# Kernel tuning notes

Measured on AMD Instinct MI355X. Metric: run time of the kernel, lower is better.

## Reference

```python
import jax, jax.numpy as jnp
import numpy as np

N = 100_000   # nodes
E = 3_200_000 # edges (avg degree 32)
F = 256       # in_features == out_features


def setup_inputs() -> dict:
    key = jax.random.key(0)
    k1, k2, k3, k4, k5, k6 = jax.random.split(key, 6)
    x = jax.random.normal(k1, (N, F), dtype=jnp.float32)
    h0 = jax.random.normal(k2, (N, F), dtype=jnp.float32)
    adj_rows = jax.random.randint(k3, (E,), 0, N, dtype=jnp.int32)
    adj_cols = jax.random.randint(k4, (E,), 0, N, dtype=jnp.int32)
    # roughly row-normalized adjacency values (avg degree 32)
    adj_vals = jax.random.uniform(k5, (E,), dtype=jnp.float32) / 32.0
    stdv = 1.0 / np.sqrt(F)
    weight = jax.random.uniform(k6, (F, F), dtype=jnp.float32, minval=-stdv, maxval=stdv)
    return {"x": x, "adj_rows": adj_rows, "adj_cols": adj_cols, "adj_vals": adj_vals,
            "h0": h0, "weight": weight, "lamda": 0.5, "alpha": 0.1, "l": 4}


def reference(x, adj_rows, adj_cols, adj_vals, h0, weight, lamda, alpha, l):
    # theta = log(lamda/l + 1)
    theta = jnp.log(jnp.float32(lamda) / l + 1.0)
    # hi = sparse.mm(adj, x): gather source rows, scale by edge value, scatter-add to dest rows
    hi = jax.ops.segment_sum(adj_vals[:, None] * x[adj_cols], adj_rows, num_segments=x.shape[0])  # [N, F]
    # support == 1 branch: affine blend with initial features h0
    support = (1.0 - alpha) * hi + alpha * h0
    # output = theta * support @ W + (1 - theta) * support   (residual=False)
    return theta * (support @ weight) + (1.0 - theta) * support
```

## Files before the change

kernel.cpp:

```cpp
#include <hip/hip_runtime.h>
#include <math.h>

#define F 256

#define BKT_SHIFT 7
#define BKT_ROWS 128
#define BKT_CAP 8192
#define NB_MAX 1024
#define BIN_CHUNK 8192

typedef __attribute__((ext_vector_type(8))) short short8;
typedef __attribute__((ext_vector_type(4))) float f32x4;
typedef __attribute__((ext_vector_type(2))) int i32x2;
typedef __attribute__((ext_vector_type(4))) unsigned short u16x4;
typedef __attribute__((ext_vector_type(8))) unsigned short u16x8;

__device__ __forceinline__ unsigned short f2bf(float f) {
  union { float f; unsigned u; } v; v.f = f;
  unsigned r = (v.u + 0x7fffu + ((v.u >> 16) & 1u)) >> 16;
  return (unsigned short)r;
}
__device__ __forceinline__ float bf2f(unsigned short h) {
  union { unsigned u; float f; } v; v.u = ((unsigned)h) << 16;
  return v.f;
}

__global__ void prep(const float* __restrict__ W, unsigned short* __restrict__ Wt,
                     const float* __restrict__ x, unsigned short* __restrict__ xb,
                     int NF, int do_xb) {
  if (blockIdx.x < 256) {
    int idx = blockIdx.x * 256 + threadIdx.x;
    int k = idx >> 8, n = idx & 255;
    Wt[n * F + k] = f2bf(W[k * F + n]);
    return;
  }
  if (!do_xb) return;
  int i0 = (blockIdx.x - 256) * 2048 + threadIdx.x * 8;
  if (i0 + 8 <= NF) {
    f32x4 a = __builtin_nontemporal_load((const f32x4*)(x + i0));
    f32x4 b = __builtin_nontemporal_load((const f32x4*)(x + i0 + 4));
    u16x8 o;
    o[0] = f2bf(a.x); o[1] = f2bf(a.y); o[2] = f2bf(a.z); o[3] = f2bf(a.w);
    o[4] = f2bf(b.x); o[5] = f2bf(b.y); o[6] = f2bf(b.z); o[7] = f2bf(b.w);
    *(u16x8*)(xb + i0) = o;
  } else {
    for (int i = i0; i < NF; ++i) xb[i] = f2bf(x[i]);
  }
}

__global__ void hist_rows(const int* __restrict__ rows, int* counts, int E) {
  int e = blockIdx.x * 256 + threadIdx.x;
  if (e < E) atomicAdd(&counts[__builtin_nontemporal_load(&rows[e])], 1);
}

__global__ void scan1(const int* __restrict__ counts, int* row_start, int* blk, int N) {
  __shared__ int tmp[256];
  int t = threadIdx.x;
  int i = blockIdx.x * 256 + t;
  int v = (i < N) ? counts[i] : 0;
  tmp[t] = v;
  __syncthreads();
#pragma unroll
  for (int off = 1; off < 256; off <<= 1) {
    int a = (t >= off) ? tmp[t - off] : 0;
    __syncthreads();
    tmp[t] += a;
    __syncthreads();
  }
  if (i < N) row_start[i] = tmp[t] - v;
  if (t == 255) blk[blockIdx.x] = tmp[255];
}

__global__ void scan2(int* blk, int NB) {
  __shared__ int tmp[512];
  int t = threadIdx.x;
  int v = (t < NB) ? blk[t] : 0;
  tmp[t] = v;
  __syncthreads();
#pragma unroll
  for (int off = 1; off < 512; off <<= 1) {
    int a = (t >= off) ? tmp[t - off] : 0;
    __syncthreads();
    tmp[t] += a;
    __syncthreads();
  }
  if (t < NB) blk[t] = tmp[t] - v;
}

__global__ void scan3(const int* __restrict__ counts, int* row_start,
                      const int* __restrict__ blk, int* fill_ptr, int N) {
  int i = blockIdx.x * 256 + threadIdx.x;
  if (i >= N) return;
  int rs = row_start[i] + blk[i >> 8];
  row_start[i] = rs;
  fill_ptr[i] = rs;
  if (i == N - 1) row_start[N] = rs + counts[i];
}

__global__ void fill_csr(const int* __restrict__ rows, const int* __restrict__ cols,
                         const float* __restrict__ vals, int* fill_ptr,
                         int2* __restrict__ edges, int E) {
  int e = blockIdx.x * 256 + threadIdx.x;
  if (e >= E) return;
  int r = __builtin_nontemporal_load(&rows[e]);
  int c = __builtin_nontemporal_load(&cols[e]);
  float v = __builtin_nontemporal_load(&vals[e]);
  int pos = atomicAdd(&fill_ptr[r], 1);
  edges[pos] = make_int2(c, __float_as_int(v));
}

__global__ __launch_bounds__(512) void bin_count(
    const int* __restrict__ rows, int* __restrict__ bucket_counts, int E, int NB) {
  __shared__ unsigned hist[NB_MAX];
  const int tid = threadIdx.x;
  const int e0 = blockIdx.x * BIN_CHUNK;
  for (int b = tid; b < NB; b += 512) hist[b] = 0;
  __syncthreads();
#pragma unroll
  for (int k = 0; k < BIN_CHUNK / 512; ++k) {
    int e = e0 + k * 512 + tid;
    if (e < E) {
      unsigned b = (unsigned)__builtin_nontemporal_load(&rows[e]) >> BKT_SHIFT;
      atomicAdd(&hist[b], 1u);
    }
  }
  __syncthreads();
  for (int b = tid; b < NB; b += 512)
    if (hist[b]) atomicAdd(&bucket_counts[b], (int)hist[b]);
}

__global__ __launch_bounds__(1024) void scan_buckets(
    const int* __restrict__ bucket_counts, int* __restrict__ bbase,
    int* __restrict__ bcur, int* __restrict__ row_start, int NB, int N, int E) {
  __shared__ int tmp[1024];
  int t = threadIdx.x;
  int v = (t < NB) ? bucket_counts[t] : 0;
  tmp[t] = v;
  __syncthreads();
#pragma unroll
  for (int off = 1; off < 1024; off <<= 1) {
    int a = (t >= off) ? tmp[t - off] : 0;
    __syncthreads();
    tmp[t] += a;
    __syncthreads();
  }
  if (t < NB) {
    int ex = tmp[t] - v;
    bbase[t] = ex;
    bcur[t] = ex;
  }
  if (t == 0) {
    bbase[NB] = E;
    row_start[N] = E;
  }
}

__global__ __launch_bounds__(512) void bin_edges(
    const int* __restrict__ rows, const int* __restrict__ cols,
    const float* __restrict__ vals, int* __restrict__ bcur,
    i32x2* __restrict__ etmp, int E, int NB) {
  __shared__ unsigned hist[NB_MAX];
  __shared__ unsigned base[NB_MAX];
  const int tid = threadIdx.x;
  const int e0 = blockIdx.x * BIN_CHUNK;

  for (int b = tid; b < NB; b += 512) hist[b] = 0;
  __syncthreads();
#pragma unroll
  for (int k = 0; k < BIN_CHUNK / 512; ++k) {
    int e = e0 + k * 512 + tid;
    if (e < E) {
      unsigned b = (unsigned)__builtin_nontemporal_load(&rows[e]) >> BKT_SHIFT;
      atomicAdd(&hist[b], 1u);
    }
  }
  __syncthreads();
  for (int b = tid; b < NB; b += 512) {
    unsigned c = hist[b];
    base[b] = c ? (unsigned)atomicAdd(&bcur[b], (int)c) : 0u;
    hist[b] = 0;
  }
  __syncthreads();
#pragma unroll
  for (int k = 0; k < BIN_CHUNK / 512; ++k) {
    int e = e0 + k * 512 + tid;
    if (e < E) {
      int r = rows[e];
      unsigned b = (unsigned)r >> BKT_SHIFT;
      unsigned idx = atomicAdd(&hist[b], 1u);
      int pos = (int)(base[b] + idx);
      int c = cols[e];
      float v = vals[e];
      etmp[pos] = (i32x2){c | ((r & (BKT_ROWS - 1)) << 20), __float_as_int(v)};
    }
  }
}

__global__ __launch_bounds__(512) void sort_bucket(
    const i32x2* __restrict__ etmp, const int* __restrict__ bbase,
    i32x2* __restrict__ edges, int* __restrict__ row_start, int N) {
  __shared__ int cur[BKT_ROWS];
  __shared__ int pre[BKT_ROWS];
  __shared__ i32x2 sorted[BKT_CAP];
  const int b = blockIdx.x;
  const int r0 = b << BKT_SHIFT;
  int nrows = N - r0; if (nrows > BKT_ROWS) nrows = BKT_ROWS;
  const int seg0 = bbase[b];
  const int cnt = bbase[b + 1] - seg0;
  const int tid = threadIdx.x;

  if (tid < BKT_ROWS) cur[tid] = 0;
  __syncthreads();
  for (int i = tid; i < cnt; i += 512) {
    i32x2 w = etmp[seg0 + i];
    atomicAdd(&cur[(w.x >> 20) & (BKT_ROWS - 1)], 1);
  }
  __syncthreads();
  int myc = (tid < BKT_ROWS) ? cur[tid] : 0;
  __syncthreads();
  for (int off = 1; off < BKT_ROWS; off <<= 1) {
    int a = 0;
    if (tid < BKT_ROWS && tid >= off) a = cur[tid - off];
    __syncthreads();
    if (tid < BKT_ROWS) cur[tid] += a;
    __syncthreads();
  }
  if (tid < BKT_ROWS) {
    int ex = cur[tid] - myc;
    pre[tid] = ex;
    cur[tid] = ex;
    if (tid < nrows) row_start[r0 + tid] = seg0 + ex;
  }
  __syncthreads();

  if (cnt <= BKT_CAP) {
    for (int i = tid; i < cnt; i += 512) {
      i32x2 w = etmp[seg0 + i];
      int rl = (w.x >> 20) & (BKT_ROWS - 1);
      int idx = atomicAdd(&cur[rl], 1);
      sorted[idx] = (i32x2){w.x & 0xFFFFF, w.y};
    }
    __syncthreads();
    for (int i = tid; i < cnt; i += 512)
      edges[seg0 + i] = sorted[i];
  } else {
    for (int i = tid; i < cnt; i += 512) {
      i32x2 w = etmp[seg0 + i];
      int rl = (w.x >> 20) & (BKT_ROWS - 1);
      int idx = atomicAdd(&cur[rl], 1);
      edges[seg0 + idx] = (i32x2){w.x & 0xFFFFF, w.y};
    }
  }
}

__global__ __launch_bounds__(256) void gather_rows_bf16(
    const unsigned short* __restrict__ xb, const float* __restrict__ h0,
    const int* __restrict__ row_start, const i32x2* __restrict__ edges,
    float* __restrict__ support, const float* __restrict__ alpha_p, int N) {
  int gid = blockIdx.x * 256 + threadIdx.x;
  int r = gid >> 6;
  if (r >= N) return;
  int lane = threadIdx.x & 63;
  float alpha = *alpha_p;
  int s = row_start[r], e = row_start[r + 1];

  const unsigned short* xbl = xb + lane * 4;

  f32x4 acc0 = (f32x4){0.f, 0.f, 0.f, 0.f};
  f32x4 acc1 = (f32x4){0.f, 0.f, 0.f, 0.f};

#define GRP_LOAD16(XV, VV, JB)                                            \
  {                                                                       \
    _Pragma("unroll")                                                     \
    for (int k = 0; k < 16; ++k) {                                        \
      int col = __builtin_amdgcn_readlane(med.x, (JB) + k);               \
      VV[k] = __int_as_float(__builtin_amdgcn_readlane(med.y, (JB) + k)); \
      XV[k] = *(const u16x4*)(xbl + (size_t)col * F);                     \
    }                                                                     \
  }

#define GRP_FMA16(XV, VV)                                                 \
  {                                                                       \
    _Pragma("unroll")                                                     \
    for (int k = 0; k < 16; ++k) {                                        \
      f32x4& A = (k & 1) ? acc1 : acc0;                                   \
      A.x += VV[k] * bf2f(XV[k][0]);                                      \
      A.y += VV[k] * bf2f(XV[k][1]);                                      \
      A.z += VV[k] * bf2f(XV[k][2]);                                      \
      A.w += VV[k] * bf2f(XV[k][3]);                                      \
    }                                                                     \
  }

  while (s < e) {
    int cnt = e - s;
    if (cnt > 64) cnt = 64;

    i32x2 med;
    if (lane < cnt) {
      med = edges[s + lane];
    } else {
      med.x = 0; med.y = 0;
    }

    u16x4 xA[16], xB[16];
    float vA[16], vB[16];

    GRP_LOAD16(xA, vA, 0);
    if (cnt > 16) GRP_LOAD16(xB, vB, 16);
    GRP_FMA16(xA, vA);
    if (cnt > 16) {
      if (cnt > 32) GRP_LOAD16(xA, vA, 32);
      GRP_FMA16(xB, vB);
      if (cnt > 32) {
        if (cnt > 48) GRP_LOAD16(xB, vB, 48);
        GRP_FMA16(xA, vA);
        if (cnt > 48) GRP_FMA16(xB, vB);
      }
    }
    s += cnt;
  }
#undef GRP_LOAD16
#undef GRP_FMA16

  f32x4 acc = acc0 + acc1;
  f32x4 b = __builtin_nontemporal_load((const f32x4*)(h0 + (size_t)r * F) + lane);
  float om = 1.0f - alpha;
  f32x4 o = om * acc + alpha * b;
  *((f32x4*)(support + (size_t)r * F) + lane) = o;
}

__global__ __launch_bounds__(256) void gather_rows_f32(
    const float* __restrict__ x, const float* __restrict__ h0,
    const int* __restrict__ row_start, const i32x2* __restrict__ edges,
    float* __restrict__ support, const float* __restrict__ alpha_p, int N) {
  int gid = blockIdx.x * 256 + threadIdx.x;
  int r = gid >> 6;
  if (r >= N) return;
  int lane = threadIdx.x & 63;
  float alpha = *alpha_p;
  int s = row_start[r], e = row_start[r + 1];
  f32x4 acc = (f32x4){0.f, 0.f, 0.f, 0.f};
  if (s < e) {
    i32x2 ed = __builtin_nontemporal_load(&edges[s]);
    f32x4 xv = *((const f32x4*)(x + (size_t)ed.x * F) + lane);
    for (int j = s; j < e; ++j) {
      i32x2 cur = ed;
      f32x4 xc = xv;
      if (j + 1 < e) {
        ed = __builtin_nontemporal_load(&edges[j + 1]);
        xv = *((const f32x4*)(x + (size_t)ed.x * F) + lane);
      }
      float v = __int_as_float(cur.y);
      acc += v * xc;
    }
  }
  f32x4 b = __builtin_nontemporal_load((const f32x4*)(h0 + (size_t)r * F) + lane);
  float om = 1.0f - alpha;
  f32x4 o = om * acc + alpha * b;
  *((f32x4*)(support + (size_t)r * F) + lane) = o;
}

__global__ __launch_bounds__(256) void gemm_epilogue(
    const float* support, const unsigned short* __restrict__ Wt, float* out,
    const float* __restrict__ lamda_p, const int* __restrict__ l_p, int N) {
  __shared__ unsigned short sup[64][264];

  const float theta = logf(*lamda_p / (float)(*l_p) + 1.0f);
  const float one_m_t = 1.0f - theta;

  const int m0 = blockIdx.x * 64;
  const int t = threadIdx.x;

#pragma unroll
  for (int i = 0; i < 16; ++i) {
    int f = t + i * 256;
    int row = f >> 6, c4 = f & 63;
    int g_row = m0 + row;
    f32x4 a = (f32x4){0.f, 0.f, 0.f, 0.f};
    if (g_row < N)
      a = __builtin_nontemporal_load((const f32x4*)(support + (size_t)g_row * F) + c4);
    unsigned short* p = &sup[row][c4 << 2];
    p[0] = f2bf(a.x); p[1] = f2bf(a.y); p[2] = f2bf(a.z); p[3] = f2bf(a.w);
  }
  __syncthreads();

  const int wave = t >> 6, lane = t & 63;
  const int quad = lane >> 4, lcol = lane & 15;
  const int mrow = wave * 16;

  f32x4 acc[16];
#pragma unroll
  for (int n = 0; n < 16; ++n) acc[n] = (f32x4){0.f, 0.f, 0.f, 0.f};

#pragma unroll
  for (int k = 0; k < 8; ++k) {
    short8 afrag = *(const short8*)&sup[mrow + lcol][k * 32 + quad * 8];
#pragma unroll
    for (int n = 0; n < 16; ++n) {
      short8 bfrag = *(const short8*)&Wt[(size_t)(n * 16 + lcol) * F + k * 32 + quad * 8];
      acc[n] = __builtin_amdgcn_mfma_f32_16x16x32_bf16(afrag, bfrag, acc[n], 0, 0, 0);
    }
  }

#pragma unroll
  for (int n = 0; n < 16; ++n) {
#pragma unroll
    for (int r = 0; r < 4; ++r) {
      int lrow = mrow + quad * 4 + r;
      int col = n * 16 + lcol;
      int g_row = m0 + lrow;
      if (g_row < N) {
        float s = bf2f(sup[lrow][col]);
        __builtin_nontemporal_store(theta * acc[n][r] + one_m_t * s,
                                    &out[(size_t)g_row * F + col]);
      }
    }
  }
}

extern "C" void kernel_launch(void* const* d_in, const int* in_sizes, int n_in,
                              void* d_out, int out_size, void* d_ws, size_t ws_size,
                              hipStream_t stream) {
  const float* x     = (const float*)d_in[0];
  const int*   rows  = (const int*)d_in[1];
  const int*   cols  = (const int*)d_in[2];
  const float* vals  = (const float*)d_in[3];
  const float* h0    = (const float*)d_in[4];
  const float* W     = (const float*)d_in[5];
  const float* lamda = (const float*)d_in[6];
  const float* alpha = (const float*)d_in[7];
  const int*   lp    = (const int*)d_in[8];

  const int E = in_sizes[1];
  const int N = in_sizes[0] / F;
  const int NF = N * F;
  const int NB = (N + BKT_ROWS - 1) >> BKT_SHIFT;

  size_t off = 0;
  auto take = [&](size_t bytes) { size_t o = off; off += (bytes + 255) & ~(size_t)255; return o; };
  char* ws = (char*)d_ws;
  unsigned short* Wt  = (unsigned short*)(ws + take((size_t)F * F * 2));
  int* counts    = (int*)(ws + take((size_t)N * 4));
  int* row_start = (int*)(ws + take((size_t)(N + 1) * 4));
  int* fill_ptr  = (int*)(ws + take((size_t)N * 4));
  int* blk       = (int*)(ws + take(4096));
  int* bucket_counts = (int*)(ws + take((size_t)NB_MAX * 4));
  int* bbase     = (int*)(ws + take((size_t)(NB_MAX + 1) * 4));
  int* bcur      = (int*)(ws + take((size_t)NB_MAX * 4));
  i32x2* edges   = (i32x2*)(ws + take((size_t)E * 8));
  unsigned short* xb = (unsigned short*)(ws + take((size_t)NF * 2));
  const int use_bf16 = (off <= ws_size);

  float* out = (float*)d_out;

  const int use_sort = (N <= (1 << 20)) && (NB <= NB_MAX) &&
                       ((size_t)E * 8 <= (size_t)out_size);

  int nxb = use_bf16 ? (NF + 2047) / 2048 : 0;
  prep<<<256 + nxb, 256, 0, stream>>>(W, Wt, x, xb, NF, use_bf16);

  int eb = (E + 255) / 256;
  int nb = (N + 255) / 256;
  int bchunks = (E + BIN_CHUNK - 1) / BIN_CHUNK;

  if (use_sort) {
    i32x2* etmp = (i32x2*)out;
    hipMemsetAsync(bucket_counts, 0, (size_t)NB * sizeof(int), stream);
    bin_count<<<bchunks, 512, 0, stream>>>(rows, bucket_counts, E, NB);
    scan_buckets<<<1, 1024, 0, stream>>>(bucket_counts, bbase, bcur, row_start,
                                         NB, N, E);
    bin_edges<<<bchunks, 512, 0, stream>>>(rows, cols, vals, bcur, etmp, E, NB);
    sort_bucket<<<NB, 512, 0, stream>>>(etmp, bbase, edges, row_start, N);
  } else {
    hipMemsetAsync(counts, 0, (size_t)N * sizeof(int), stream);
    hist_rows<<<eb, 256, 0, stream>>>(rows, counts, E);
    scan1<<<nb, 256, 0, stream>>>(counts, row_start, blk, N);
    scan2<<<1, 512, 0, stream>>>(blk, nb);
    scan3<<<nb, 256, 0, stream>>>(counts, row_start, blk, fill_ptr, N);
    fill_csr<<<eb, 256, 0, stream>>>(rows, cols, vals, fill_ptr, (int2*)edges, E);
  }

  int gather_blocks = (N * 64 + 255) / 256;
  if (use_bf16) {
    gather_rows_bf16<<<gather_blocks, 256, 0, stream>>>(xb, h0, row_start, edges,
                                                        out, alpha, N);
  } else {
    gather_rows_f32<<<gather_blocks, 256, 0, stream>>>(x, h0, row_start, edges,
                                                       out, alpha, N);
  }

  gemm_epilogue<<<(N + 63) / 64, 256, 0, stream>>>(out, Wt, out, lamda, lp, N);
}
```

Measured before the change: 711.6 us.

## Fuse bucket sort with row gather and fold bucket counting into prep

Shrinks buckets to 32 rows and fuses the per-bucket local sort directly into the SpMM gather kernel. Each wave accumulates four rows from the LDS-sorted edge list, so the sorted edges are never written back and the separate gather pass is gone. The bucket histogram now runs as extra blocks of the prep launch, removing one kernel, and the gather inner loop uses smaller 8-wide software-pipelined groups. In exchange there are more buckets and a multi-pass scan, and each block handles only 32 rows with serial chunking for overflow, which may lower parallelism per row.

```diff
diff --git a/kernel.cpp b/kernel.cpp
--- a/kernel.cpp
+++ b/kernel.cpp
@@ -3,11 +3,11 @@
 
 #define F 256
 
-#define BKT_SHIFT 7
-#define BKT_ROWS 128
-#define BKT_CAP 8192
-#define NB_MAX 1024
-#define BIN_CHUNK 8192
+#define SBKT_SHIFT 5
+#define SBKT_ROWS 32
+#define SBKT_CAP 2048
+#define NB_MAX 4096
+#define BIN_CHUNK 16384
 
 typedef __attribute__((ext_vector_type(8))) short short8;
 typedef __attribute__((ext_vector_type(4))) float f32x4;
@@ -27,24 +27,237 @@
 
 __global__ void prep(const float* __restrict__ W, unsigned short* __restrict__ Wt,
                      const float* __restrict__ x, unsigned short* __restrict__ xb,
-                     int NF, int do_xb) {
+                     int NF, const int* __restrict__ rows,
+                     int* __restrict__ bucket_counts, int nxb, int E, int NB) {
   if (blockIdx.x < 256) {
     int idx = blockIdx.x * 256 + threadIdx.x;
     int k = idx >> 8, n = idx & 255;
     Wt[n * F + k] = f2bf(W[k * F + n]);
     return;
   }
-  if (!do_xb) return;
-  int i0 = (blockIdx.x - 256) * 2048 + threadIdx.x * 8;
-  if (i0 + 8 <= NF) {
-    f32x4 a = __builtin_nontemporal_load((const f32x4*)(x + i0));
-    f32x4 b = __builtin_nontemporal_load((const f32x4*)(x + i0 + 4));
-    u16x8 o;
-    o[0] = f2bf(a.x); o[1] = f2bf(a.y); o[2] = f2bf(a.z); o[3] = f2bf(a.w);
-    o[4] = f2bf(b.x); o[5] = f2bf(b.y); o[6] = f2bf(b.z); o[7] = f2bf(b.w);
-    *(u16x8*)(xb + i0) = o;
-  } else {
-    for (int i = i0; i < NF; ++i) xb[i] = f2bf(x[i]);
+  int xbid = blockIdx.x - 256;
+  if (xbid < nxb) {
+    int i0 = xbid * 2048 + threadIdx.x * 8;
+    if (i0 + 8 <= NF) {
+      f32x4 a = __builtin_nontemporal_load((const f32x4*)(x + i0));
+      f32x4 b = __builtin_nontemporal_load((const f32x4*)(x + i0 + 4));
+      u16x8 o;
+      o[0] = f2bf(a.x); o[1] = f2bf(a.y); o[2] = f2bf(a.z); o[3] = f2bf(a.w);
+      o[4] = f2bf(b.x); o[5] = f2bf(b.y); o[6] = f2bf(b.z); o[7] = f2bf(b.w);
+      *(u16x8*)(xb + i0) = o;
+    } else {
+      for (int i = i0; i < NF; ++i) xb[i] = f2bf(x[i]);
+    }
+    return;
+  }
+  __shared__ unsigned hist[NB_MAX];
+  const int tid = threadIdx.x;
+  const int e0 = (xbid - nxb) * BIN_CHUNK;
+  for (int b = tid; b < NB; b += 256) hist[b] = 0;
+  __syncthreads();
+  for (int k = 0; k < BIN_CHUNK / 256; ++k) {
+    int e = e0 + k * 256 + tid;
+    if (e < E) {
+      unsigned b = (unsigned)__builtin_nontemporal_load(&rows[e]) >> SBKT_SHIFT;
+      atomicAdd(&hist[b], 1u);
+    }
+  }
+  __syncthreads();
+  for (int b = tid; b < NB; b += 256)
+    if (hist[b]) atomicAdd(&bucket_counts[b], (int)hist[b]);
+}
+
+__global__ __launch_bounds__(1024) void scan_buckets(
+    const int* __restrict__ bucket_counts, int* __restrict__ bbase,
+    int* __restrict__ bcur, int NB, int E) {
+  __shared__ int tmp[1024];
+  int t = threadIdx.x;
+  int carry = 0;
+  for (int c0 = 0; c0 < NB; c0 += 1024) {
+    int idx = c0 + t;
+    int v = (idx < NB) ? bucket_counts[idx] : 0;
+    tmp[t] = v;
+    __syncthreads();
+#pragma unroll
+    for (int off = 1; off < 1024; off <<= 1) {
+      int a = (t >= off) ? tmp[t - off] : 0;
+      __syncthreads();
+      tmp[t] += a;
+      __syncthreads();
+    }
+    if (idx < NB) {
+      int ex = carry + tmp[t] - v;
+      bbase[idx] = ex;
+      bcur[idx] = ex;
+    }
+    carry += tmp[1023];
+    __syncthreads();
+  }
+  if (t == 0) bbase[NB] = E;
+}
+
+__global__ __launch_bounds__(512) void bin_edges(
+    const int* __restrict__ rows, const int* __restrict__ cols,
+    const float* __restrict__ vals, int* __restrict__ bcur,
+    i32x2* __restrict__ ebin, int E, int NB) {
+  __shared__ unsigned hist[NB_MAX];
+  __shared__ unsigned base[NB_MAX];
+  const int tid = threadIdx.x;
+  const int e0 = blockIdx.x * BIN_CHUNK;
+
+  for (int b = tid; b < NB; b += 512) hist[b] = 0;
+  __syncthreads();
+  for (int k = 0; k < BIN_CHUNK / 512; ++k) {
+    int e = e0 + k * 512 + tid;
+    if (e < E) {
+      unsigned b = (unsigned)__builtin_nontemporal_load(&rows[e]) >> SBKT_SHIFT;
+      atomicAdd(&hist[b], 1u);
+    }
+  }
+  __syncthreads();
+  for (int b = tid; b < NB; b += 512) {
+    unsigned c = hist[b];
+    base[b] = c ? (unsigned)atomicAdd(&bcur[b], (int)c) : 0u;
+    hist[b] = 0;
+  }
+  __syncthreads();
+  for (int k = 0; k < BIN_CHUNK / 512; ++k) {
+    int e = e0 + k * 512 + tid;
+    if (e < E) {
+      int r = rows[e];
+      unsigned b = (unsigned)r >> SBKT_SHIFT;
+      unsigned idx = atomicAdd(&hist[b], 1u);
+      int pos = (int)(base[b] + idx);
+      int c = cols[e];
+      float v = vals[e];
+      ebin[pos] = (i32x2){c | ((r & (SBKT_ROWS - 1)) << 20), __float_as_int(v)};
+    }
+  }
+}
+
+__global__ __launch_bounds__(512) void sort_gather(
+    const i32x2* __restrict__ ebin, const int* __restrict__ bbase,
+    const unsigned short* __restrict__ xb, const float* __restrict__ h0,
+    float* __restrict__ out, const float* __restrict__ alpha_p, int N) {
+  __shared__ int cur[SBKT_ROWS];
+  __shared__ int pre[SBKT_ROWS + 1];
+  __shared__ i32x2 sorted[SBKT_CAP];
+  const int b = blockIdx.x;
+  const int r0 = b << SBKT_SHIFT;
+  const int tid = threadIdx.x;
+  const int wave = tid >> 6, lane = tid & 63;
+  const float alpha = *alpha_p;
+  int seg = bbase[b];
+  const int segend = bbase[b + 1];
+  const unsigned short* xbl = xb + lane * 4;
+
+  f32x4 accA[4], accB[4];
+#pragma unroll
+  for (int q = 0; q < 4; ++q) {
+    accA[q] = (f32x4){0.f, 0.f, 0.f, 0.f};
+    accB[q] = (f32x4){0.f, 0.f, 0.f, 0.f};
+  }
+
+#define GRP_LOAD(XV, VV, JB)                                              \
+  {                                                                       \
+    _Pragma("unroll")                                                     \
+    for (int k = 0; k < 8; ++k) {                                         \
+      int col = __builtin_amdgcn_readlane(med.x, (JB) + k);               \
+      VV[k] = __int_as_float(__builtin_amdgcn_readlane(med.y, (JB) + k)); \
+      XV[k] = *(const u16x4*)(xbl + (size_t)col * F);                     \
+    }                                                                     \
+  }
+
+#define GRP_FMA(XV, VV, AA, AB)                                           \
+  {                                                                       \
+    _Pragma("unroll")                                                     \
+    for (int k = 0; k < 8; ++k) {                                         \
+      f32x4& A = (k & 1) ? AB : AA;                                       \
+      A.x += VV[k] * bf2f(XV[k][0]);                                      \
+      A.y += VV[k] * bf2f(XV[k][1]);                                      \
+      A.z += VV[k] * bf2f(XV[k][2]);                                      \
+      A.w += VV[k] * bf2f(XV[k][3]);                                      \
+    }                                                                     \
+  }
+
+  while (seg < segend) {
+    int cnt = segend - seg;
+    if (cnt > SBKT_CAP) cnt = SBKT_CAP;
+
+    if (tid < SBKT_ROWS) cur[tid] = 0;
+    __syncthreads();
+    for (int i = tid; i < cnt; i += 512)
+      atomicAdd(&cur[(ebin[seg + i].x >> 20) & (SBKT_ROWS - 1)], 1);
+    __syncthreads();
+    int myc = (tid < SBKT_ROWS) ? cur[tid] : 0;
+    __syncthreads();
+#pragma unroll
+    for (int off = 1; off < SBKT_ROWS; off <<= 1) {
+      int a = (tid < SBKT_ROWS && tid >= off) ? cur[tid - off] : 0;
+      __syncthreads();
+      if (tid < SBKT_ROWS) cur[tid] += a;
+      __syncthreads();
+    }
+    if (tid < SBKT_ROWS) {
+      int ex = cur[tid] - myc;
+      pre[tid] = ex;
+      cur[tid] = ex;
+      if (tid == SBKT_ROWS - 1) pre[SBKT_ROWS] = cnt;
+    }
+    __syncthreads();
+    for (int i = tid; i < cnt; i += 512) {
+      i32x2 w = ebin[seg + i];
+      int rl = (w.x >> 20) & (SBKT_ROWS - 1);
+      int idx = atomicAdd(&cur[rl], 1);
+      sorted[idx] = (i32x2){w.x & 0xFFFFF, w.y};
+    }
+    __syncthreads();
+
+#pragma unroll
+    for (int q = 0; q < 4; ++q) {
+      int rho = (wave << 2) + q;
+      int s = pre[rho], e2 = pre[rho + 1];
+      while (s < e2) {
+        int c64 = e2 - s;
+        if (c64 > 64) c64 = 64;
+        i32x2 med;
+        if (lane < c64) med = sorted[s + lane];
+        else { med.x = 0; med.y = 0; }
+
+        u16x4 xA[8], xB[8];
+        float vA[8], vB[8];
+        int jb = 0;
+        GRP_LOAD(xA, vA, 0);
+        while (true) {
+          int jn = jb + 8;
+          if (jn < c64) GRP_LOAD(xB, vB, jn);
+          GRP_FMA(xA, vA, accA[q], accB[q]);
+          jb = jn;
+          if (jb >= c64) break;
+          jn = jb + 8;
+          if (jn < c64) GRP_LOAD(xA, vA, jn);
+          GRP_FMA(xB, vB, accA[q], accB[q]);
+          jb = jn;
+          if (jb >= c64) break;
+        }
+        s += c64;
+      }
+    }
+    seg += cnt;
+    __syncthreads();
+  }
+#undef GRP_LOAD
+#undef GRP_FMA
+
+  const float om = 1.0f - alpha;
+#pragma unroll
+  for (int q = 0; q < 4; ++q) {
+    int r = r0 + (wave << 2) + q;
+    if (r < N) {
+      f32x4 bb = __builtin_nontemporal_load((const f32x4*)(h0 + (size_t)r * F) + lane);
+      f32x4 o = om * (accA[q] + accB[q]) + alpha * bb;
+      *((f32x4*)(out + (size_t)r * F) + lane) = o;
+    }
   }
 }
 
@@ -109,150 +322,6 @@
   edges[pos] = make_int2(c, __float_as_int(v));
 }
 
-__global__ __launch_bounds__(512) void bin_count(
-    const int* __restrict__ rows, int* __restrict__ bucket_counts, int E, int NB) {
-  __shared__ unsigned hist[NB_MAX];
-  const int tid = threadIdx.x;
-  const int e0 = blockIdx.x * BIN_CHUNK;
-  for (int b = tid; b < NB; b += 512) hist[b] = 0;
-  __syncthreads();
-#pragma unroll
-  for (int k = 0; k < BIN_CHUNK / 512; ++k) {
-    int e = e0 + k * 512 + tid;
-    if (e < E) {
-      unsigned b = (unsigned)__builtin_nontemporal_load(&rows[e]) >> BKT_SHIFT;
-      atomicAdd(&hist[b], 1u);
-    }
-  }
-  __syncthreads();
-  for (int b = tid; b < NB; b += 512)
-    if (hist[b]) atomicAdd(&bucket_counts[b], (int)hist[b]);
-}
-
-__global__ __launch_bounds__(1024) void scan_buckets(
-    const int* __restrict__ bucket_counts, int* __restrict__ bbase,
-    int* __restrict__ bcur, int* __restrict__ row_start, int NB, int N, int E) {
-  __shared__ int tmp[1024];
-  int t = threadIdx.x;
-  int v = (t < NB) ? bucket_counts[t] : 0;
-  tmp[t] = v;
-  __syncthreads();
-#pragma unroll
-  for (int off = 1; off < 1024; off <<= 1) {
-    int a = (t >= off) ? tmp[t - off] : 0;
-    __syncthreads();
-    tmp[t] += a;
-    __syncthreads();
-  }
-  if (t < NB) {
-    int ex = tmp[t] - v;
-    bbase[t] = ex;
-    bcur[t] = ex;
-  }
-  if (t == 0) {
-    bbase[NB] = E;
-    row_start[N] = E;
-  }
-}
-
-__global__ __launch_bounds__(512) void bin_edges(
-    const int* __restrict__ rows, const int* __restrict__ cols,
-    const float* __restrict__ vals, int* __restrict__ bcur,
-    i32x2* __restrict__ etmp, int E, int NB) {
-  __shared__ unsigned hist[NB_MAX];
-  __shared__ unsigned base[NB_MAX];
-  const int tid = threadIdx.x;
-  const int e0 = blockIdx.x * BIN_CHUNK;
-
-  for (int b = tid; b < NB; b += 512) hist[b] = 0;
-  __syncthreads();
-#pragma unroll
-  for (int k = 0; k < BIN_CHUNK / 512; ++k) {
-    int e = e0 + k * 512 + tid;
-    if (e < E) {
-      unsigned b = (unsigned)__builtin_nontemporal_load(&rows[e]) >> BKT_SHIFT;
-      atomicAdd(&hist[b], 1u);
-    }
-  }
-  __syncthreads();
-  for (int b = tid; b < NB; b += 512) {
-    unsigned c = hist[b];
-    base[b] = c ? (unsigned)atomicAdd(&bcur[b], (int)c) : 0u;
-    hist[b] = 0;
-  }
-  __syncthreads();
-#pragma unroll
-  for (int k = 0; k < BIN_CHUNK / 512; ++k) {
-    int e = e0 + k * 512 + tid;
-    if (e < E) {
-      int r = rows[e];
-      unsigned b = (unsigned)r >> BKT_SHIFT;
-      unsigned idx = atomicAdd(&hist[b], 1u);
-      int pos = (int)(base[b] + idx);
-      int c = cols[e];
-      float v = vals[e];
-      etmp[pos] = (i32x2){c | ((r & (BKT_ROWS - 1)) << 20), __float_as_int(v)};
-    }
-  }
-}
-
-__global__ __launch_bounds__(512) void sort_bucket(
-    const i32x2* __restrict__ etmp, const int* __restrict__ bbase,
-    i32x2* __restrict__ edges, int* __restrict__ row_start, int N) {
-  __shared__ int cur[BKT_ROWS];
-  __shared__ int pre[BKT_ROWS];
-  __shared__ i32x2 sorted[BKT_CAP];
-  const int b = blockIdx.x;
-  const int r0 = b << BKT_SHIFT;
-  int nrows = N - r0; if (nrows > BKT_ROWS) nrows = BKT_ROWS;
-  const int seg0 = bbase[b];
-  const int cnt = bbase[b + 1] - seg0;
-  const int tid = threadIdx.x;
-
-  if (tid < BKT_ROWS) cur[tid] = 0;
-  __syncthreads();
-  for (int i = tid; i < cnt; i += 512) {
-    i32x2 w = etmp[seg0 + i];
-    atomicAdd(&cur[(w.x >> 20) & (BKT_ROWS - 1)], 1);
-  }
-  __syncthreads();
-  int myc = (tid < BKT_ROWS) ? cur[tid] : 0;
-  __syncthreads();
-  for (int off = 1; off < BKT_ROWS; off <<= 1) {
-    int a = 0;
-    if (tid < BKT_ROWS && tid >= off) a = cur[tid - off];
-    __syncthreads();
-    if (tid < BKT_ROWS) cur[tid] += a;
-    __syncthreads();
-  }
-  if (tid < BKT_ROWS) {
-    int ex = cur[tid] - myc;
-    pre[tid] = ex;
-    cur[tid] = ex;
-    if (tid < nrows) row_start[r0 + tid] = seg0 + ex;
-  }
-  __syncthreads();
-
-  if (cnt <= BKT_CAP) {
-    for (int i = tid; i < cnt; i += 512) {
-      i32x2 w = etmp[seg0 + i];
-      int rl = (w.x >> 20) & (BKT_ROWS - 1);
-      int idx = atomicAdd(&cur[rl], 1);
-      sorted[idx] = (i32x2){w.x & 0xFFFFF, w.y};
-    }
-    __syncthreads();
-    for (int i = tid; i < cnt; i += 512)
-      edges[seg0 + i] = sorted[i];
-  } else {
-    for (int i = tid; i < cnt; i += 512) {
-      i32x2 w = etmp[seg0 + i];
-      int rl = (w.x >> 20) & (BKT_ROWS - 1);
-      int idx = atomicAdd(&cur[rl], 1);
-      edges[seg0 + idx] = (i32x2){w.x & 0xFFFFF, w.y};
-    }
-  }
-}
-
 __global__ __launch_bounds__(256) void gather_rows_bf16(
     const unsigned short* __restrict__ xb, const float* __restrict__ h0,
     const int* __restrict__ row_start, const i32x2* __restrict__ edges,
@@ -263,26 +332,23 @@
   int lane = threadIdx.x & 63;
   float alpha = *alpha_p;
   int s = row_start[r], e = row_start[r + 1];
-
   const unsigned short* xbl = xb + lane * 4;
-
   f32x4 acc0 = (f32x4){0.f, 0.f, 0.f, 0.f};
   f32x4 acc1 = (f32x4){0.f, 0.f, 0.f, 0.f};
 
-#define GRP_LOAD16(XV, VV, JB)                                            \
+#define GRP_LOAD8(XV, VV, JB)                                             \
   {                                                                       \
     _Pragma("unroll")                                                     \
-    for (int k = 0; k < 16; ++k) {                                        \
+    for (int k = 0; k < 8; ++k) {                                         \
       int col = __builtin_amdgcn_readlane(med.x, (JB) + k);               \
       VV[k] = __int_as_float(__builtin_amdgcn_readlane(med.y, (JB) + k)); \
       XV[k] = *(const u16x4*)(xbl + (size_t)col * F);                     \
     }                                                                     \
   }
-
-#define GRP_FMA16(XV, VV)                                                 \
+#define GRP_FMA8(XV, VV)                                                  \
   {                                                                       \
     _Pragma("unroll")                                                     \
-    for (int k = 0; k < 16; ++k) {                                        \
+    for (int k = 0; k < 8; ++k) {                                         \
       f32x4& A = (k & 1) ? acc1 : acc0;                                   \
       A.x += VV[k] * bf2f(XV[k][0]);                                      \
       A.y += VV[k] * bf2f(XV[k][1]);                                      \
@@ -294,33 +360,29 @@
   while (s < e) {
     int cnt = e - s;
     if (cnt > 64) cnt = 64;
-
     i32x2 med;
-    if (lane < cnt) {
-      med = edges[s + lane];
-    } else {
-      med.x = 0; med.y = 0;
-    }
-
-    u16x4 xA[16], xB[16];
-    float vA[16], vB[16];
-
-    GRP_LOAD16(xA, vA, 0);
-    if (cnt > 16) GRP_LOAD16(xB, vB, 16);
-    GRP_FMA16(xA, vA);
-    if (cnt > 16) {
-      if (cnt > 32) GRP_LOAD16(xA, vA, 32);
-      GRP_FMA16(xB, vB);
-      if (cnt > 32) {
-        if (cnt > 48) GRP_LOAD16(xB, vB, 48);
-        GRP_FMA16(xA, vA);
-        if (cnt > 48) GRP_FMA16(xB, vB);
-      }
+    if (lane < cnt) med = edges[s + lane];
+    else { med.x = 0; med.y = 0; }
+    u16x4 xA[8], xB[8];
+    float vA[8], vB[8];
+    int jb = 0;
+    GRP_LOAD8(xA, vA, 0);
+    while (true) {
+      int jn = jb + 8;
+      if (jn < cnt) GRP_LOAD8(xB, vB, jn);
+      GRP_FMA8(xA, vA);
+      jb = jn;
+      if (jb >= cnt) break;
+      jn = jb + 8;
+      if (jn < cnt) GRP_LOAD8(xA, vA, jn);
+      GRP_FMA8(xB, vB);
+      jb = jn;
+      if (jb >= cnt) break;
     }
     s += cnt;
   }
-#undef GRP_LOAD16
-#undef GRP_FMA16
+#undef GRP_LOAD8
+#undef GRP_FMA8
 
   f32x4 acc = acc0 + acc1;
   f32x4 b = __builtin_nontemporal_load((const f32x4*)(h0 + (size_t)r * F) + lane);
@@ -434,7 +496,7 @@
   const int E = in_sizes[1];
   const int N = in_sizes[0] / F;
   const int NF = N * F;
-  const int NB = (N + BKT_ROWS - 1) >> BKT_SHIFT;
+  const int NB = (N + SBKT_ROWS - 1) >> SBKT_SHIFT;
 
   size_t off = 0;
   auto take = [&](size_t bytes) { size_t o = off; off += (bytes + 255) & ~(size_t)255; return o; };
@@ -453,40 +515,37 @@
 
   float* out = (float*)d_out;
 
-  const int use_sort = (N <= (1 << 20)) && (NB <= NB_MAX) &&
-                       ((size_t)E * 8 <= (size_t)out_size);
+  const int use_sort = use_bf16 && (E > 0) && (N <= (1 << 20)) && (NB <= NB_MAX);
 
   int nxb = use_bf16 ? (NF + 2047) / 2048 : 0;
-  prep<<<256 + nxb, 256, 0, stream>>>(W, Wt, x, xb, NF, use_bf16);
-
   int eb = (E + 255) / 256;
   int nb = (N + 255) / 256;
   int bchunks = (E + BIN_CHUNK - 1) / BIN_CHUNK;
 
   if (use_sort) {
-    i32x2* etmp = (i32x2*)out;
     hipMemsetAsync(bucket_counts, 0, (size_t)NB * sizeof(int), stream);
-    bin_count<<<bchunks, 512, 0, stream>>>(rows, bucket_counts, E, NB);
-    scan_buckets<<<1, 1024, 0, stream>>>(bucket_counts, bbase, bcur, row_start,
-                                         NB, N, E);
-    bin_edges<<<bchunks, 512, 0, stream>>>(rows, cols, vals, bcur, etmp, E, NB);
-    sort_bucket<<<NB, 512, 0, stream>>>(etmp, bbase, edges, row_start, N);
+    prep<<<256 + nxb + bchunks, 256, 0, stream>>>(W, Wt, x, xb, NF, rows,
+                                                  bucket_counts, nxb, E, NB);
+    scan_buckets<<<1, 1024, 0, stream>>>(bucket_counts, bbase, bcur, NB, E);
+    bin_edges<<<bchunks, 512, 0, stream>>>(rows, cols, vals, bcur, edges, E, NB);
+    sort_gather<<<NB, 512, 0, stream>>>(edges, bbase, xb, h0, out, alpha, N);
   } else {
+    prep<<<256 + nxb, 256, 0, stream>>>(W, Wt, x, xb, NF, rows,
+                                        bucket_counts, nxb, E, 0);
     hipMemsetAsync(counts, 0, (size_t)N * sizeof(int), stream);
     hist_rows<<<eb, 256, 0, stream>>>(rows, counts, E);
     scan1<<<nb, 256, 0, stream>>>(counts, row_start, blk, N);
     scan2<<<1, 512, 0, stream>>>(blk, nb);
     scan3<<<nb, 256, 0, stream>>>(counts, row_start, blk, fill_ptr, N);
     fill_csr<<<eb, 256, 0, stream>>>(rows, cols, vals, fill_ptr, (int2*)edges, E);
-  }
-
-  int gather_blocks = (N * 64 + 255) / 256;
-  if (use_bf16) {
-    gather_rows_bf16<<<gather_blocks, 256, 0, stream>>>(xb, h0, row_start, edges,
-                                                        out, alpha, N);
-  } else {
-    gather_rows_f32<<<gather_blocks, 256, 0, stream>>>(x, h0, row_start, edges,
-                                                       out, alpha, N);
+    int gather_blocks = (N * 64 + 255) / 256;
+    if (use_bf16) {
+      gather_rows_bf16<<<gather_blocks, 256, 0, stream>>>(xb, h0, row_start, edges,
+                                                          out, alpha, N);
+    } else {
+      gather_rows_f32<<<gather_blocks, 256, 0, stream>>>(x, h0, row_start, edges,
+                                                         out, alpha, N);
+    }
   }
 
   gemm_epilogue<<<(N + 63) / 64, 256, 0, stream>>>(out, Wt, out, lamda, lp, N);
```

Measured after the change: 777.3 us. 9.2% more time.

## Fuse bucket histogram into prep, use per-chunk offsets, store support in bf16

Applied to the files above, without the earlier changes.

Bucket counting moves into the prep kernel as extra blocks that write a per-chunk histogram matrix. A single scan kernel turns that matrix into deterministic per-chunk write offsets. This removes the memset, the separate bin_count kernel, the recount in bin_edges and its global atomics. The gather now writes the support matrix as bf16 to workspace so the GEMM reads half the bytes. It also shrinks the gather's edge-group unroll from 16 to 8 with a ping-pong loop. The cost is extra workspace and an O(chunks) serial loop per bucket in the scan.

```diff
diff --git a/kernel.cpp b/kernel.cpp
--- a/kernel.cpp
+++ b/kernel.cpp
@@ -27,171 +27,95 @@
 
 __global__ void prep(const float* __restrict__ W, unsigned short* __restrict__ Wt,
                      const float* __restrict__ x, unsigned short* __restrict__ xb,
-                     int NF, int do_xb) {
+                     int NF, const int* __restrict__ rows,
+                     int* __restrict__ hist_mat, int nxb, int E, int NB) {
   if (blockIdx.x < 256) {
     int idx = blockIdx.x * 256 + threadIdx.x;
     int k = idx >> 8, n = idx & 255;
     Wt[n * F + k] = f2bf(W[k * F + n]);
     return;
   }
-  if (!do_xb) return;
-  int i0 = (blockIdx.x - 256) * 2048 + threadIdx.x * 8;
-  if (i0 + 8 <= NF) {
-    f32x4 a = __builtin_nontemporal_load((const f32x4*)(x + i0));
-    f32x4 b = __builtin_nontemporal_load((const f32x4*)(x + i0 + 4));
-    u16x8 o;
-    o[0] = f2bf(a.x); o[1] = f2bf(a.y); o[2] = f2bf(a.z); o[3] = f2bf(a.w);
-    o[4] = f2bf(b.x); o[5] = f2bf(b.y); o[6] = f2bf(b.z); o[7] = f2bf(b.w);
-    *(u16x8*)(xb + i0) = o;
-  } else {
-    for (int i = i0; i < NF; ++i) xb[i] = f2bf(x[i]);
-  }
-}
-
-__global__ void hist_rows(const int* __restrict__ rows, int* counts, int E) {
-  int e = blockIdx.x * 256 + threadIdx.x;
-  if (e < E) atomicAdd(&counts[__builtin_nontemporal_load(&rows[e])], 1);
-}
-
-__global__ void scan1(const int* __restrict__ counts, int* row_start, int* blk, int N) {
-  __shared__ int tmp[256];
+  int xbid = blockIdx.x - 256;
+  if (xbid < nxb) {
+    int i0 = xbid * 2048 + threadIdx.x * 8;
+    if (i0 + 8 <= NF) {
+      f32x4 a = __builtin_nontemporal_load((const f32x4*)(x + i0));
+      f32x4 b = __builtin_nontemporal_load((const f32x4*)(x + i0 + 4));
+      u16x8 o;
+      o[0] = f2bf(a.x); o[1] = f2bf(a.y); o[2] = f2bf(a.z); o[3] = f2bf(a.w);
+      o[4] = f2bf(b.x); o[5] = f2bf(b.y); o[6] = f2bf(b.z); o[7] = f2bf(b.w);
+      *(u16x8*)(xb + i0) = o;
+    } else {
+      for (int i = i0; i < NF; ++i) xb[i] = f2bf(x[i]);
+    }
+    return;
+  }
+  __shared__ int hist[NB_MAX];
+  const int tid = threadIdx.x;
+  const int c = xbid - nxb;
+  const int e0 = c * BIN_CHUNK;
+  for (int b = tid; b < NB; b += 256) hist[b] = 0;
+  __syncthreads();
+#pragma unroll
+  for (int k = 0; k < BIN_CHUNK / 256; ++k) {
+    int e = e0 + k * 256 + tid;
+    if (e < E) atomicAdd(&hist[rows[e] >> BKT_SHIFT], 1);
+  }
+  __syncthreads();
+  for (int b = tid; b < NB; b += 256) hist_mat[c * NB + b] = hist[b];
+}
+
+__global__ __launch_bounds__(1024) void scan_buckets(
+    int* __restrict__ hm, int* __restrict__ bbase, int* __restrict__ row_start,
+    int nch, int NB, int E, int N) {
+  __shared__ int tot[1024];
   int t = threadIdx.x;
-  int i = blockIdx.x * 256 + t;
-  int v = (i < N) ? counts[i] : 0;
-  tmp[t] = v;
-  __syncthreads();
-#pragma unroll
-  for (int off = 1; off < 256; off <<= 1) {
-    int a = (t >= off) ? tmp[t - off] : 0;
-    __syncthreads();
-    tmp[t] += a;
-    __syncthreads();
-  }
-  if (i < N) row_start[i] = tmp[t] - v;
-  if (t == 255) blk[blockIdx.x] = tmp[255];
-}
-
-__global__ void scan2(int* blk, int NB) {
-  __shared__ int tmp[512];
-  int t = threadIdx.x;
-  int v = (t < NB) ? blk[t] : 0;
-  tmp[t] = v;
-  __syncthreads();
-#pragma unroll
-  for (int off = 1; off < 512; off <<= 1) {
-    int a = (t >= off) ? tmp[t - off] : 0;
-    __syncthreads();
-    tmp[t] += a;
-    __syncthreads();
-  }
-  if (t < NB) blk[t] = tmp[t] - v;
-}
-
-__global__ void scan3(const int* __restrict__ counts, int* row_start,
-                      const int* __restrict__ blk, int* fill_ptr, int N) {
-  int i = blockIdx.x * 256 + threadIdx.x;
-  if (i >= N) return;
-  int rs = row_start[i] + blk[i >> 8];
-  row_start[i] = rs;
-  fill_ptr[i] = rs;
-  if (i == N - 1) row_start[N] = rs + counts[i];
-}
-
-__global__ void fill_csr(const int* __restrict__ rows, const int* __restrict__ cols,
-                         const float* __restrict__ vals, int* fill_ptr,
-                         int2* __restrict__ edges, int E) {
-  int e = blockIdx.x * 256 + threadIdx.x;
-  if (e >= E) return;
-  int r = __builtin_nontemporal_load(&rows[e]);
-  int c = __builtin_nontemporal_load(&cols[e]);
-  float v = __builtin_nontemporal_load(&vals[e]);
-  int pos = atomicAdd(&fill_ptr[r], 1);
-  edges[pos] = make_int2(c, __float_as_int(v));
-}
-
-__global__ __launch_bounds__(512) void bin_count(
-    const int* __restrict__ rows, int* __restrict__ bucket_counts, int E, int NB) {
-  __shared__ unsigned hist[NB_MAX];
-  const int tid = threadIdx.x;
-  const int e0 = blockIdx.x * BIN_CHUNK;
-  for (int b = tid; b < NB; b += 512) hist[b] = 0;
-  __syncthreads();
-#pragma unroll
-  for (int k = 0; k < BIN_CHUNK / 512; ++k) {
-    int e = e0 + k * 512 + tid;
-    if (e < E) {
-      unsigned b = (unsigned)__builtin_nontemporal_load(&rows[e]) >> BKT_SHIFT;
-      atomicAdd(&hist[b], 1u);
-    }
-  }
-  __syncthreads();
-  for (int b = tid; b < NB; b += 512)
-    if (hist[b]) atomicAdd(&bucket_counts[b], (int)hist[b]);
-}
-
-__global__ __launch_bounds__(1024) void scan_buckets(
-    const int* __restrict__ bucket_counts, int* __restrict__ bbase,
-    int* __restrict__ bcur, int* __restrict__ row_start, int NB, int N, int E) {
-  __shared__ int tmp[1024];
-  int t = threadIdx.x;
-  int v = (t < NB) ? bucket_counts[t] : 0;
-  tmp[t] = v;
-  __syncthreads();
-#pragma unroll
+  int total_b = 0;
+  if (t < NB) {
+    int run = 0;
+    for (int c = 0; c < nch; ++c) {
+      int v = hm[c * NB + t];
+      hm[c * NB + t] = run;
+      run += v;
+    }
+    total_b = run;
+  }
+  tot[t] = (t < NB) ? total_b : 0;
+  __syncthreads();
   for (int off = 1; off < 1024; off <<= 1) {
-    int a = (t >= off) ? tmp[t - off] : 0;
-    __syncthreads();
-    tmp[t] += a;
+    int a = (t >= off) ? tot[t - off] : 0;
+    __syncthreads();
+    tot[t] += a;
     __syncthreads();
   }
   if (t < NB) {
-    int ex = tmp[t] - v;
+    int ex = tot[t] - total_b;
     bbase[t] = ex;
-    bcur[t] = ex;
-  }
-  if (t == 0) {
-    bbase[NB] = E;
-    row_start[N] = E;
-  }
+    for (int c = 0; c < nch; ++c) hm[c * NB + t] += ex;
+  }
+  if (t == 0) { bbase[NB] = E; row_start[N] = E; }
 }
 
 __global__ __launch_bounds__(512) void bin_edges(
     const int* __restrict__ rows, const int* __restrict__ cols,
-    const float* __restrict__ vals, int* __restrict__ bcur,
+    const float* __restrict__ vals, const int* __restrict__ hm,
     i32x2* __restrict__ etmp, int E, int NB) {
-  __shared__ unsigned hist[NB_MAX];
-  __shared__ unsigned base[NB_MAX];
+  __shared__ int cur[NB_MAX];
   const int tid = threadIdx.x;
-  const int e0 = blockIdx.x * BIN_CHUNK;
-
-  for (int b = tid; b < NB; b += 512) hist[b] = 0;
-  __syncthreads();
-#pragma unroll
-  for (int k = 0; k < BIN_CHUNK / 512; ++k) {
-    int e = e0 + k * 512 + tid;
-    if (e < E) {
-      unsigned b = (unsigned)__builtin_nontemporal_load(&rows[e]) >> BKT_SHIFT;
-      atomicAdd(&hist[b], 1u);
-    }
-  }
-  __syncthreads();
-  for (int b = tid; b < NB; b += 512) {
-    unsigned c = hist[b];
-    base[b] = c ? (unsigned)atomicAdd(&bcur[b], (int)c) : 0u;
-    hist[b] = 0;
-  }
+  const int c = blockIdx.x;
+  const int e0 = c * BIN_CHUNK;
+  for (int b = tid; b < NB; b += 512) cur[b] = hm[c * NB + b];
   __syncthreads();
 #pragma unroll
   for (int k = 0; k < BIN_CHUNK / 512; ++k) {
     int e = e0 + k * 512 + tid;
     if (e < E) {
       int r = rows[e];
-      unsigned b = (unsigned)r >> BKT_SHIFT;
-      unsigned idx = atomicAdd(&hist[b], 1u);
-      int pos = (int)(base[b] + idx);
-      int c = cols[e];
-      float v = vals[e];
-      etmp[pos] = (i32x2){c | ((r & (BKT_ROWS - 1)) << 20), __float_as_int(v)};
+      int b = r >> BKT_SHIFT;
+      int pos = atomicAdd(&cur[b], 1);
+      int cc = __builtin_nontemporal_load(&cols[e]);
+      float v = __builtin_nontemporal_load(&vals[e]);
+      etmp[pos] = (i32x2){cc | ((r & (BKT_ROWS - 1)) << 20), __float_as_int(v)};
     }
   }
 }
@@ -211,10 +135,8 @@
 
   if (tid < BKT_ROWS) cur[tid] = 0;
   __syncthreads();
-  for (int i = tid; i < cnt; i += 512) {
-    i32x2 w = etmp[seg0 + i];
-    atomicAdd(&cur[(w.x >> 20) & (BKT_ROWS - 1)], 1);
-  }
+  for (int i = tid; i < cnt; i += 512)
+    atomicAdd(&cur[(etmp[seg0 + i].x >> 20) & (BKT_ROWS - 1)], 1);
   __syncthreads();
   int myc = (tid < BKT_ROWS) ? cur[tid] : 0;
   __syncthreads();
@@ -256,33 +178,31 @@
 __global__ __launch_bounds__(256) void gather_rows_bf16(
     const unsigned short* __restrict__ xb, const float* __restrict__ h0,
     const int* __restrict__ row_start, const i32x2* __restrict__ edges,
-    float* __restrict__ support, const float* __restrict__ alpha_p, int N) {
+    float* __restrict__ outf32, unsigned short* __restrict__ sup16,
+    const float* __restrict__ alpha_p, int N, int use16) {
   int gid = blockIdx.x * 256 + threadIdx.x;
   int r = gid >> 6;
   if (r >= N) return;
   int lane = threadIdx.x & 63;
   float alpha = *alpha_p;
   int s = row_start[r], e = row_start[r + 1];
-
   const unsigned short* xbl = xb + lane * 4;
-
   f32x4 acc0 = (f32x4){0.f, 0.f, 0.f, 0.f};
   f32x4 acc1 = (f32x4){0.f, 0.f, 0.f, 0.f};
 
-#define GRP_LOAD16(XV, VV, JB)                                            \
+#define GRP_LOAD8(XV, VV, JB)                                             \
   {                                                                       \
     _Pragma("unroll")                                                     \
-    for (int k = 0; k < 16; ++k) {                                        \
+    for (int k = 0; k < 8; ++k) {                                         \
       int col = __builtin_amdgcn_readlane(med.x, (JB) + k);               \
       VV[k] = __int_as_float(__builtin_amdgcn_readlane(med.y, (JB) + k)); \
       XV[k] = *(const u16x4*)(xbl + (size_t)col * F);                     \
     }                                                                     \
   }
-
-#define GRP_FMA16(XV, VV)                                                 \
+#define GRP_FMA8(XV, VV)                                                  \
   {                                                                       \
     _Pragma("unroll")                                                     \
-    for (int k = 0; k < 16; ++k) {                                        \
+    for (int k = 0; k < 8; ++k) {                                         \
       f32x4& A = (k & 1) ? acc1 : acc0;                                   \
       A.x += VV[k] * bf2f(XV[k][0]);                                      \
       A.y += VV[k] * bf2f(XV[k][1]);                                      \
@@ -294,39 +214,41 @@
   while (s < e) {
     int cnt = e - s;
     if (cnt > 64) cnt = 64;
-
     i32x2 med;
-    if (lane < cnt) {
-      med = edges[s + lane];
-    } else {
-      med.x = 0; med.y = 0;
-    }
-
-    u16x4 xA[16], xB[16];
-    float vA[16], vB[16];
-
-    GRP_LOAD16(xA, vA, 0);
-    if (cnt > 16) GRP_LOAD16(xB, vB, 16);
-    GRP_FMA16(xA, vA);
-    if (cnt > 16) {
-      if (cnt > 32) GRP_LOAD16(xA, vA, 32);
-      GRP_FMA16(xB, vB);
-      if (cnt > 32) {
-        if (cnt > 48) GRP_LOAD16(xB, vB, 48);
-        GRP_FMA16(xA, vA);
-        if (cnt > 48) GRP_FMA16(xB, vB);
-      }
+    if (lane < cnt) med = edges[s + lane];
+    else { med.x = 0; med.y = 0; }
+    u16x4 xA[8], xB[8];
+    float vA[8], vB[8];
+    int jb = 0;
+    GRP_LOAD8(xA, vA, 0);
+    while (true) {
+      int jn = jb + 8;
+      if (jn < cnt) GRP_LOAD8(xB, vB, jn);
+      GRP_FMA8(xA, vA);
+      jb = jn;
+      if (jb >= cnt) break;
+      jn = jb + 8;
+      if (jn < cnt) GRP_LOAD8(xA, vA, jn);
+      GRP_FMA8(xB, vB);
+      jb = jn;
+      if (jb >= cnt) break;
     }
     s += cnt;
   }
-#undef GRP_LOAD16
-#undef GRP_FMA16
+#undef GRP_LOAD8
+#undef GRP_FMA8
 
   f32x4 acc = acc0 + acc1;
   f32x4 b = __builtin_nontemporal_load((const f32x4*)(h0 + (size_t)r * F) + lane);
   float om = 1.0f - alpha;
   f32x4 o = om * acc + alpha * b;
-  *((f32x4*)(support + (size_t)r * F) + lane) = o;
+  if (use16) {
+    u16x4 ov;
+    ov[0] = f2bf(o.x); ov[1] = f2bf(o.y); ov[2] = f2bf(o.z); ov[3] = f2bf(o.w);
+    *(u16x4*)(sup16 + (size_t)r * F + lane * 4) = ov;
+  } else {
+    *((f32x4*)(outf32 + (size_t)r * F) + lane) = o;
+  }
 }
 
 __global__ __launch_bounds__(256) void gather_rows_f32(
@@ -361,8 +283,10 @@
 }
 
 __global__ __launch_bounds__(256) void gemm_epilogue(
-    const float* support, const unsigned short* __restrict__ Wt, float* out,
-    const float* __restrict__ lamda_p, const int* __restrict__ l_p, int N) {
+    const float* support, const unsigned short* __restrict__ sup16,
+    const unsigned short* __restrict__ Wt, float* out,
+    const float* __restrict__ lamda_p, const int* __restrict__ l_p,
+    int N, int use16) {
   __shared__ unsigned short sup[64][264];
 
   const float theta = logf(*lamda_p / (float)(*l_p) + 1.0f);
@@ -371,16 +295,29 @@
   const int m0 = blockIdx.x * 64;
   const int t = threadIdx.x;
 
-#pragma unroll
-  for (int i = 0; i < 16; ++i) {
-    int f = t + i * 256;
-    int row = f >> 6, c4 = f & 63;
-    int g_row = m0 + row;
-    f32x4 a = (f32x4){0.f, 0.f, 0.f, 0.f};
-    if (g_row < N)
-      a = __builtin_nontemporal_load((const f32x4*)(support + (size_t)g_row * F) + c4);
-    unsigned short* p = &sup[row][c4 << 2];
-    p[0] = f2bf(a.x); p[1] = f2bf(a.y); p[2] = f2bf(a.z); p[3] = f2bf(a.w);
+  if (use16) {
+#pragma unroll
+    for (int i = 0; i < 8; ++i) {
+      int g = t + i * 256;
+      int row = g >> 5, c8 = g & 31;
+      int g_row = m0 + row;
+      u16x8 v = (u16x8){0, 0, 0, 0, 0, 0, 0, 0};
+      if (g_row < N)
+        v = *(const u16x8*)(sup16 + (size_t)g_row * F + c8 * 8);
+      *(u16x8*)&sup[row][c8 << 3] = v;
+    }
+  } else {
+#pragma unroll
+    for (int i = 0; i < 16; ++i) {
+      int f = t + i * 256;
+      int row = f >> 6, c4 = f & 63;
+      int g_row = m0 + row;
+      f32x4 a = (f32x4){0.f, 0.f, 0.f, 0.f};
+      if (g_row < N)
+        a = __builtin_nontemporal_load((const f32x4*)(support + (size_t)g_row * F) + c4);
+      unsigned short* p = &sup[row][c4 << 2];
+      p[0] = f2bf(a.x); p[1] = f2bf(a.y); p[2] = f2bf(a.z); p[3] = f2bf(a.w);
+    }
   }
   __syncthreads();
 
@@ -416,6 +353,67 @@
       }
     }
   }
+}
+
+__global__ void hist_rows(const int* __restrict__ rows, int* counts, int E) {
+  int e = blockIdx.x * 256 + threadIdx.x;
+  if (e < E) atomicAdd(&counts[__builtin_nontemporal_load(&rows[e])], 1);
+}
+
+__global__ void scan1(const int* __restrict__ counts, int* row_start, int* blk, int N) {
+  __shared__ int tmp[256];
+  int t = threadIdx.x;
+  int i = blockIdx.x * 256 + t;
+  int v = (i < N) ? counts[i] : 0;
+  tmp[t] = v;
+  __syncthreads();
+#pragma unroll
+  for (int off = 1; off < 256; off <<= 1) {
+    int a = (t >= off) ? tmp[t - off] : 0;
+    __syncthreads();
+    tmp[t] += a;
+    __syncthreads();
+  }
+  if (i < N) row_start[i] = tmp[t] - v;
+  if (t == 255) blk[blockIdx.x] = tmp[255];
+}
+
+__global__ void scan2(int* blk, int NB) {
+  __shared__ int tmp[512];
+  int t = threadIdx.x;
+  int v = (t < NB) ? blk[t] : 0;
+  tmp[t] = v;
+  __syncthreads();
+#pragma unroll
+  for (int off = 1; off < 512; off <<= 1) {
+    int a = (t >= off) ? tmp[t - off] : 0;
+    __syncthreads();
+    tmp[t] += a;
+    __syncthreads();
+  }
+  if (t < NB) blk[t] = tmp[t] - v;
+}
+
+__global__ void scan3(const int* __restrict__ counts, int* row_start,
+                      const int* __restrict__ blk, int* fill_ptr, int N) {
+  int i = blockIdx.x * 256 + threadIdx.x;
+  if (i >= N) return;
+  int rs = row_start[i] + blk[i >> 8];
+  row_start[i] = rs;
+  fill_ptr[i] = rs;
+  if (i == N - 1) row_start[N] = rs + counts[i];
+}
+
+__global__ void fill_csr(const int* __restrict__ rows, const int* __restrict__ cols,
+                         const float* __restrict__ vals, int* fill_ptr,
+                         int2* __restrict__ edges, int E) {
+  int e = blockIdx.x * 256 + threadIdx.x;
+  if (e >= E) return;
+  int r = __builtin_nontemporal_load(&rows[e]);
+  int c = __builtin_nontemporal_load(&cols[e]);
+  float v = __builtin_nontemporal_load(&vals[e]);
+  int pos = atomicAdd(&fill_ptr[r], 1);
+  edges[pos] = make_int2(c, __float_as_int(v));
 }
 
 extern "C" void kernel_launch(void* const* d_in, const int* in_sizes, int n_in,
@@ -435,6 +433,7 @@
   const int N = in_sizes[0] / F;
   const int NF = N * F;
   const int NB = (N + BKT_ROWS - 1) >> BKT_SHIFT;
+  const int bchunks = (E + BIN_CHUNK - 1) / BIN_CHUNK;
 
   size_t off = 0;
   auto take = [&](size_t bytes) { size_t o = off; off += (bytes + 255) & ~(size_t)255; return o; };
@@ -444,50 +443,53 @@
   int* row_start = (int*)(ws + take((size_t)(N + 1) * 4));
   int* fill_ptr  = (int*)(ws + take((size_t)N * 4));
   int* blk       = (int*)(ws + take(4096));
-  int* bucket_counts = (int*)(ws + take((size_t)NB_MAX * 4));
   int* bbase     = (int*)(ws + take((size_t)(NB_MAX + 1) * 4));
-  int* bcur      = (int*)(ws + take((size_t)NB_MAX * 4));
+  int* hist_mat  = (int*)(ws + take((size_t)bchunks * NB * 4));
   i32x2* edges   = (i32x2*)(ws + take((size_t)E * 8));
   unsigned short* xb = (unsigned short*)(ws + take((size_t)NF * 2));
   const int use_bf16 = (off <= ws_size);
+  unsigned short* sup16 = (unsigned short*)(ws + take((size_t)NF * 2));
+  const int use_sup16 = (off <= ws_size);
 
   float* out = (float*)d_out;
 
-  const int use_sort = (N <= (1 << 20)) && (NB <= NB_MAX) &&
+  const int use_sort = use_bf16 && (E > 0) && (N <= (1 << 20)) && (NB <= NB_MAX) &&
                        ((size_t)E * 8 <= (size_t)out_size);
 
   int nxb = use_bf16 ? (NF + 2047) / 2048 : 0;
-  prep<<<256 + nxb, 256, 0, stream>>>(W, Wt, x, xb, NF, use_bf16);
-
   int eb = (E + 255) / 256;
   int nb = (N + 255) / 256;
-  int bchunks = (E + BIN_CHUNK - 1) / BIN_CHUNK;
 
   if (use_sort) {
     i32x2* etmp = (i32x2*)out;
-    hipMemsetAsync(bucket_counts, 0, (size_t)NB * sizeof(int), stream);
-    bin_count<<<bchunks, 512, 0, stream>>>(rows, bucket_counts, E, NB);
-    scan_buckets<<<1, 1024, 0, stream>>>(bucket_counts, bbase, bcur, row_start,
-                                         NB, N, E);
-    bin_edges<<<bchunks, 512, 0, stream>>>(rows, cols, vals, bcur, etmp, E, NB);
+    prep<<<256 + nxb + bchunks, 256, 0, stream>>>(W, Wt, x, xb, NF, rows,
+                                                  hist_mat, nxb, E, NB);
+    scan_buckets<<<1, 1024, 0, stream>>>(hist_mat, bbase, row_start, bchunks, NB, E, N);
+    bin_edges<<<bchunks, 512, 0, stream>>>(rows, cols, vals, hist_mat, etmp, E, NB);
     sort_bucket<<<NB, 512, 0, stream>>>(etmp, bbase, edges, row_start, N);
+    int gather_blocks = (N * 64 + 255) / 256;
+    gather_rows_bf16<<<gather_blocks, 256, 0, stream>>>(
+        xb, h0, row_start, edges, out, sup16, alpha, N, use_sup16);
+    gemm_epilogue<<<(N + 63) / 64, 256, 0, stream>>>(
+        out, sup16, Wt, out, lamda, lp, N, use_sup16);
   } else {
+    prep<<<256 + nxb, 256, 0, stream>>>(W, Wt, x, xb, NF, rows,
+                                        hist_mat, nxb, E, 0);
     hipMemsetAsync(counts, 0, (size_t)N * sizeof(int), stream);
     hist_rows<<<eb, 256, 0, stream>>>(rows, counts, E);
     scan1<<<nb, 256, 0, stream>>>(counts, row_start, blk, N);
     scan2<<<1, 512, 0, stream>>>(blk, nb);
     scan3<<<nb, 256, 0, stream>>>(counts, row_start, blk, fill_ptr, N);
     fill_csr<<<eb, 256, 0, stream>>>(rows, cols, vals, fill_ptr, (int2*)edges, E);
-  }
-
-  int gather_blocks = (N * 64 + 255) / 256;
-  if (use_bf16) {
-    gather_rows_bf16<<<gather_blocks, 256, 0, stream>>>(xb, h0, row_start, edges,
-                                                        out, alpha, N);
-  } else {
-    gather_rows_f32<<<gather_blocks, 256, 0, stream>>>(x, h0, row_start, edges,
-                                                       out, alpha, N);
-  }
-
-  gemm_epilogue<<<(N + 63) / 64, 256, 0, stream>>>(out, Wt, out, lamda, lp, N);
-}
+    int gather_blocks = (N * 64 + 255) / 256;
+    if (use_bf16) {
+      gather_rows_bf16<<<gather_blocks, 256, 0, stream>>>(
+          xb, h0, row_start, edges, out, sup16, alpha, N, 0);
+    } else {
+      gather_rows_f32<<<gather_blocks, 256, 0, stream>>>(x, h0, row_start, edges,
+                                                         out, alpha, N);
+    }
+    gemm_epilogue<<<(N + 63) / 64, 256, 0, stream>>>(
+        out, sup16, Wt, out, lamda, lp, N, 0);
+  }
+}
```

Result: slower. 828.8 us (+16.5%).
